# Kernel optimization log

Hardware: AMD Instinct MI355X
Metric: run time of the kernel (lower is better)

Reference implementation:

```python
import jax, jax.numpy as jnp
import numpy as np
import math

D_MODEL = 1024
N_HEADS = 16
SEQ = 1024
BATCH = 4


def setup_inputs() -> dict:
    key = jax.random.key(0)
    ks = jax.random.split(key, 13)
    s = 1.0 / math.sqrt(D_MODEL)  # keep logits in a sane range
    return {
        "x": jax.random.normal(ks[0], (BATCH, SEQ, D_MODEL), jnp.float32),
        "Wq": jax.random.normal(ks[1], (D_MODEL, D_MODEL), jnp.float32) * s,
        "bq": jnp.zeros((D_MODEL,), jnp.float32),
        "Wk": jax.random.normal(ks[2], (D_MODEL, D_MODEL), jnp.float32) * s,
        "bk": jnp.zeros((D_MODEL,), jnp.float32),
        "Wv": jax.random.normal(ks[3], (D_MODEL, D_MODEL), jnp.float32) * s,
        "bv": jnp.zeros((D_MODEL,), jnp.float32),
        "Wo": jax.random.normal(ks[4], (D_MODEL, D_MODEL), jnp.float32) * s,
        "bo": jnp.zeros((D_MODEL,), jnp.float32),
        "Wimp": jax.random.normal(ks[5], (N_HEADS, D_MODEL), jnp.float32) * s,
        "bimp": jnp.zeros((N_HEADS,), jnp.float32),
        "k_ema": jax.random.normal(ks[6], (SEQ, D_MODEL), jnp.float32),
        "v_ema": jax.random.normal(ks[7], (SEQ, D_MODEL), jnp.float32),
    }


def reference(x, Wq, bq, Wk, bk, Wv, bv, Wo, bo, Wimp, bimp, k_ema, v_ema):
    B, S, D = x.shape
    H = Wimp.shape[0]
    hd = D // H

    def proj(W, b):
        # [B,S,D] -> [B,H,S,hd]
        return (x @ W.T + b).reshape(B, S, H, hd).transpose(0, 2, 1, 3)

    q = proj(Wq, bq)
    k = proj(Wk, bk)
    v = proj(Wv, bv)

    scores = jnp.einsum("bhqd,bhkd->bhqk", q, k) / math.sqrt(hd)

    # importance bias: outer-sum of per-head key/value importance vectors
    k_imp = (k_ema[:S] @ Wimp.T + bimp).T  # [H, S]
    v_imp = (v_ema[:S] @ Wimp.T + bimp).T  # [H, S]
    bias = 0.5 * (k_imp[:, :, None] + v_imp[:, None, :])  # [H, S, S]
    scores = scores + 0.1 * bias[None]

    # causal mask (torch masks before bias add; -inf + finite == -inf, so equivalent)
    causal = jnp.triu(jnp.ones((S, S), bool), k=1)
    scores = jnp.where(causal, -jnp.inf, scores)

    attn = jax.nn.softmax(scores, axis=-1)
    out = jnp.einsum("bhqk,bhkd->bhqd", attn, v)
    out = out.transpose(0, 2, 1, 3).reshape(B, S, D)
    return out @ Wo.T + bo
```

## Files before the change

kernel.cpp:

```cpp
#include <hip/hip_runtime.h>
#include <hip/hip_bf16.h>
#include <math.h>

#define D_MODEL 1024
#define SEQ     1024
#define BATCH   4
#define NHEADS  16
#define HD      64

#define QSC 0.18033688f
#define BSC 0.072134752f

typedef __bf16 bf16x8 __attribute__((ext_vector_type(8)));
typedef __bf16 bf16x4 __attribute__((ext_vector_type(4)));
typedef float  f32x4  __attribute__((ext_vector_type(4)));

__device__ __forceinline__ f32x4 mfma16(bf16x8 a, bf16x8 b, f32x4 c) {
  return __builtin_amdgcn_mfma_f32_16x16x32_bf16(a, b, c, 0, 0, 0);
}

__device__ __forceinline__ void async16(__bf16* lds, const __bf16* g) {
  __builtin_amdgcn_global_load_lds(g, lds, 16, 0, 0);
}

__device__ __forceinline__ float fexp2(float x) {
  float r;
  asm volatile("v_exp_f32 %0, %1" : "=v"(r) : "v"(x));
  return r;
}

__global__ __launch_bounds__(256) void prep_kernel(
    const float* __restrict__ x,
    const float* __restrict__ Wq, const float* __restrict__ Wk,
    const float* __restrict__ Wv, const float* __restrict__ Wo,
    const float* __restrict__ v_ema,
    const float* __restrict__ Wimp, const float* __restrict__ bimp,
    __bf16* __restrict__ x_bf, __bf16* __restrict__ wq_bf, __bf16* __restrict__ wk_bf,
    __bf16* __restrict__ wv_bf, __bf16* __restrict__ wo_bf,
    float* __restrict__ vimp) {
  const int bid = blockIdx.x;
  const int tid = threadIdx.x;
  if (bid < 4096) {
    int i = bid * 256 + tid;
    float4 v = ((const float4*)x)[i];
    bf16x4 o; o[0] = (__bf16)v.x; o[1] = (__bf16)v.y; o[2] = (__bf16)v.z; o[3] = (__bf16)v.w;
    ((bf16x4*)x_bf)[i] = o;
  } else if (bid < 8192) {
    int i = (bid - 4096) * 256 + tid;
    int sel = i >> 18;
    int j = i & 262143;
    const float* s = (sel == 0) ? Wq : (sel == 1) ? Wk : (sel == 2) ? Wv : Wo;
    __bf16* d      = (sel == 0) ? wq_bf : (sel == 1) ? wk_bf : (sel == 2) ? wv_bf : wo_bf;
    float4 v = ((const float4*)s)[j];
    bf16x4 o; o[0] = (__bf16)v.x; o[1] = (__bf16)v.y; o[2] = (__bf16)v.z; o[3] = (__bf16)v.w;
    ((bf16x4*)d)[j] = o;
  } else {
    const int s    = (bid - 8192) * 4 + (tid >> 6);
    const int lane = tid & 63;
    const float4* ve = (const float4*)(v_ema + (size_t)s * D_MODEL);
    float acc0 = 0.f, acc1 = 0.f, acc2 = 0.f, acc3 = 0.f;
    float acc4 = 0.f, acc5 = 0.f, acc6 = 0.f, acc7 = 0.f;
    float acc8 = 0.f, acc9 = 0.f, accA = 0.f, accB = 0.f;
    float accC = 0.f, accD = 0.f, accE = 0.f, accF = 0.f;
    #pragma unroll
    for (int i = 0; i < 4; i++) {
      const int c = lane + i * 64;
      float4 v = ve[c];
      #define VIMP_H(H, ACC)                                                     \
        {                                                                        \
          float4 w = ((const float4*)(Wimp + (H) * D_MODEL))[c];                 \
          ACC += v.x * w.x + v.y * w.y + v.z * w.z + v.w * w.w;                  \
        }
      VIMP_H(0, acc0)  VIMP_H(1, acc1)  VIMP_H(2, acc2)  VIMP_H(3, acc3)
      VIMP_H(4, acc4)  VIMP_H(5, acc5)  VIMP_H(6, acc6)  VIMP_H(7, acc7)
      VIMP_H(8, acc8)  VIMP_H(9, acc9)  VIMP_H(10, accA) VIMP_H(11, accB)
      VIMP_H(12, accC) VIMP_H(13, accD) VIMP_H(14, accE) VIMP_H(15, accF)
      #undef VIMP_H
    }
    #define VIMP_RED(ACC)                                                        \
      for (int mm = 32; mm >= 1; mm >>= 1) ACC += __shfl_xor(ACC, mm);
    VIMP_RED(acc0) VIMP_RED(acc1) VIMP_RED(acc2) VIMP_RED(acc3)
    VIMP_RED(acc4) VIMP_RED(acc5) VIMP_RED(acc6) VIMP_RED(acc7)
    VIMP_RED(acc8) VIMP_RED(acc9) VIMP_RED(accA) VIMP_RED(accB)
    VIMP_RED(accC) VIMP_RED(accD) VIMP_RED(accE) VIMP_RED(accF)
    #undef VIMP_RED
    if (lane == 0) {
      vimp[0  * SEQ + s] = acc0 + bimp[0];  vimp[1  * SEQ + s] = acc1 + bimp[1];
      vimp[2  * SEQ + s] = acc2 + bimp[2];  vimp[3  * SEQ + s] = acc3 + bimp[3];
      vimp[4  * SEQ + s] = acc4 + bimp[4];  vimp[5  * SEQ + s] = acc5 + bimp[5];
      vimp[6  * SEQ + s] = acc6 + bimp[6];  vimp[7  * SEQ + s] = acc7 + bimp[7];
      vimp[8  * SEQ + s] = acc8 + bimp[8];  vimp[9  * SEQ + s] = acc9 + bimp[9];
      vimp[10 * SEQ + s] = accA + bimp[10]; vimp[11 * SEQ + s] = accB + bimp[11];
      vimp[12 * SEQ + s] = accC + bimp[12]; vimp[13 * SEQ + s] = accD + bimp[13];
      vimp[14 * SEQ + s] = accE + bimp[14]; vimp[15 * SEQ + s] = accF + bimp[15];
    }
  }
}

__global__ __launch_bounds__(256) void gemm_qkv(
    const __bf16* __restrict__ A,
    const __bf16* __restrict__ Wq, const __bf16* __restrict__ Wk, const __bf16* __restrict__ Wv,
    const float* __restrict__ bq, const float* __restrict__ bk, const float* __restrict__ bv,
    __bf16* __restrict__ qo, __bf16* __restrict__ kp, __bf16* __restrict__ vp) {
  const int id = blockIdx.x + (blockIdx.y << 4);
  const int xcd = id & 7;
  const int j = id >> 3;
  const int by = (j & 3) * 8 + xcd;
  const int bx = j >> 2;

  __shared__ __bf16 As[2 * 8192];
  __shared__ __bf16 Ws[3][2 * 4096];

  const int tid = threadIdx.x;
  const int w = tid >> 6, l = tid & 63;
  const int quad = l >> 4, l16 = l & 15;
  const int wy = w >> 1, wx = w & 1;
  const int row0 = by * 128;
  const int col0 = bx * 64;

  const f32x4 fzero = {0.f, 0.f, 0.f, 0.f};
  f32x4 aq[4][2], ak[4][2], av[4][2];
  #pragma unroll
  for (int i = 0; i < 4; i++)
    #pragma unroll
    for (int jj = 0; jj < 2; jj++) { aq[i][jj] = fzero; ak[i][jj] = fzero; av[i][jj] = fzero; }

  const int rk = tid >> 3;
  const int csw = (((tid & 7) ^ (rk & 7)) * 8);
  const int tid8 = tid * 8;
  const __bf16* aS = A  + (size_t)(row0 + rk) * D_MODEL + csw;
  const __bf16* qS = Wq + (size_t)(col0 + rk) * D_MODEL + csw;
  const __bf16* kS = Wk + (size_t)(col0 + rk) * D_MODEL + csw;
  const __bf16* vS = Wv + (size_t)(col0 + rk) * D_MODEL + csw;

  const int pch0 = ((0 * 4 + quad) ^ (l16 & 7)) * 8;
  const int pch1 = ((1 * 4 + quad) ^ (l16 & 7)) * 8;

  #pragma unroll
  for (int p = 0; p < 4; ++p)
    async16(&As[p * 2048 + tid8], aS + (size_t)p * 32 * D_MODEL);
  #pragma unroll
  for (int p = 0; p < 2; ++p) {
    async16(&Ws[0][p * 2048 + tid8], qS + (size_t)p * 32 * D_MODEL);
    async16(&Ws[1][p * 2048 + tid8], kS + (size_t)p * 32 * D_MODEL);
    async16(&Ws[2][p * 2048 + tid8], vS + (size_t)p * 32 * D_MODEL);
  }

  #pragma unroll 2
  for (int t = 0; t < 16; ++t) {
    const int rbA = (t & 1) << 13;
    const int rbW = (t & 1) << 12;
    if (t < 15) {
      const int sbA = ((t + 1) & 1) << 13;
      const int sbW = ((t + 1) & 1) << 12;
      const size_t kk = (size_t)(t + 1) * 64;
      #pragma unroll
      for (int p = 0; p < 4; ++p)
        async16(&As[sbA + p * 2048 + tid8], aS + (size_t)p * 32 * D_MODEL + kk);
      #pragma unroll
      for (int p = 0; p < 2; ++p) {
        async16(&Ws[0][sbW + p * 2048 + tid8], qS + (size_t)p * 32 * D_MODEL + kk);
        async16(&Ws[1][sbW + p * 2048 + tid8], kS + (size_t)p * 32 * D_MODEL + kk);
        async16(&Ws[2][sbW + p * 2048 + tid8], vS + (size_t)p * 32 * D_MODEL + kk);
      }
      asm volatile("s_waitcnt vmcnt(10)" ::: "memory");
    } else {
      asm volatile("s_waitcnt vmcnt(0)" ::: "memory");
    }
    __builtin_amdgcn_s_barrier();
    #pragma unroll
    for (int ks = 0; ks < 2; ++ks) {
      const int pch = ks ? pch1 : pch0;
      bf16x8 af[4], qf[2], kf[2], vf[2];
      #pragma unroll
      for (int mi = 0; mi < 4; mi++)
        af[mi] = *(const bf16x8*)&As[rbA + (wy * 64 + mi * 16 + l16) * 64 + pch];
      #pragma unroll
      for (int ni = 0; ni < 2; ni++) {
        const int wrow = (wx * 32 + ni * 16 + l16) * 64 + pch;
        qf[ni] = *(const bf16x8*)&Ws[0][rbW + wrow];
        kf[ni] = *(const bf16x8*)&Ws[1][rbW + wrow];
        vf[ni] = *(const bf16x8*)&Ws[2][rbW + wrow];
      }
      #pragma unroll
      for (int mi = 0; mi < 4; mi++)
        #pragma unroll
        for (int ni = 0; ni < 2; ni++) {
          aq[mi][ni] = mfma16(af[mi], qf[ni], aq[mi][ni]);
          ak[mi][ni] = mfma16(kf[ni], af[mi], ak[mi][ni]);
          av[mi][ni] = mfma16(af[mi], vf[ni], av[mi][ni]);
        }
    }
    __builtin_amdgcn_s_barrier();
  }

  #pragma unroll
  for (int ni = 0; ni < 2; ni++) {
    const int col = col0 + wx * 32 + ni * 16 + l16;
    const float bqv = bq[col];
    #pragma unroll
    for (int mi = 0; mi < 4; mi++) {
      const int row = row0 + wy * 64 + mi * 16 + quad * 4;
      #pragma unroll
      for (int r = 0; r < 4; r++)
        qo[(size_t)(row + r) * D_MODEL + col] = (__bf16)((aq[mi][ni][r] + bqv) * QSC);
    }
  }
  #pragma unroll
  for (int ni = 0; ni < 2; ni++) {
    const int wcolbase = col0 + wx * 32 + ni * 16 + quad * 4;
    const float4 b4 = *(const float4*)&bk[wcolbase];
    const float bb[4] = {b4.x, b4.y, b4.z, b4.w};
    #pragma unroll
    for (int mi = 0; mi < 4; mi++) {
      const int token = row0 + wy * 64 + mi * 16 + l16;
      const int bh = (token >> 10) * 16 + (wcolbase >> 6);
      const int colp = ((wcolbase & 63) + ((token & 7) << 3)) & 63;
      union { __bf16 hh[4]; uint2 uu; } pk;
      #pragma unroll
      for (int r = 0; r < 4; r++) pk.hh[r] = (__bf16)(ak[mi][ni][r] + bb[r]);
      *(uint2*)(kp + ((size_t)bh * SEQ + (token & 1023)) * HD + colp) = pk.uu;
    }
  }
  #pragma unroll
  for (int ni = 0; ni < 2; ni++) {
    const int col = col0 + wx * 32 + ni * 16 + l16;
    const float bvv = bv[col];
    #pragma unroll
    for (int mi = 0; mi < 4; mi++) {
      const int token = row0 + wy * 64 + mi * 16 + quad * 4;
      const int bh = (token >> 10) * 16 + (col >> 6);
      const int chk = (token >> 6) & 15;
      const int keyp = ((token & 63) + ((col & 7) << 3)) & 63;
      const size_t base = (((size_t)bh * 16 + chk) * 64 + (col & 63)) * 64 + keyp;
      union { __bf16 hh[4]; uint2 uu; } pk;
      #pragma unroll
      for (int r = 0; r < 4; r++) pk.hh[r] = (__bf16)(av[mi][ni][r] + bvv);
      *(uint2*)(vp + base) = pk.uu;
    }
  }
}

__global__ __launch_bounds__(256) void gemm_o(
    const __bf16* __restrict__ A, const __bf16* __restrict__ W,
    const float* __restrict__ bias, float* __restrict__ out) {
  const int id = blockIdx.x + (blockIdx.y << 4);
  const int xcd = id & 7;
  const int j = id >> 3;
  const int by = (j & 3) * 8 + xcd;
  const int bx = j >> 2;

  __shared__ __bf16 As[2 * 8192];
  __shared__ __bf16 Bs[2 * 4096];

  const int tid = threadIdx.x;
  const int w = tid >> 6, l = tid & 63;
  const int quad = l >> 4, l16 = l & 15;
  const int wy = w >> 1, wx = w & 1;
  const int row0 = by * 128;
  const int col0 = bx * 64;

  const f32x4 fzero = {0.f, 0.f, 0.f, 0.f};
  f32x4 acc[4][2];
  for (int i = 0; i < 4; i++)
    for (int jj = 0; jj < 2; jj++) acc[i][jj] = fzero;

  const int rk = tid >> 3;
  const int csw = (((tid & 7) ^ (rk & 7)) * 8);
  const int tid8 = tid * 8;
  const __bf16* aS = A + (size_t)(row0 + rk) * D_MODEL + csw;
  const __bf16* bS = W + (size_t)(col0 + rk) * D_MODEL + csw;

  const int pch0 = ((0 * 4 + quad) ^ (l16 & 7)) * 8;
  const int pch1 = ((1 * 4 + quad) ^ (l16 & 7)) * 8;

  #pragma unroll
  for (int p = 0; p < 4; ++p)
    async16(&As[p * 2048 + tid8], aS + (size_t)p * 32 * D_MODEL);
  #pragma unroll
  for (int p = 0; p < 2; ++p)
    async16(&Bs[p * 2048 + tid8], bS + (size_t)p * 32 * D_MODEL);

  #pragma unroll 2
  for (int t = 0; t < 16; ++t) {
    const int rbA = (t & 1) << 13;
    const int rbB = (t & 1) << 12;
    if (t < 15) {
      const int sbA = ((t + 1) & 1) << 13;
      const int sbB = ((t + 1) & 1) << 12;
      const size_t kk = (size_t)(t + 1) * 64;
      #pragma unroll
      for (int p = 0; p < 4; ++p)
        async16(&As[sbA + p * 2048 + tid8], aS + (size_t)p * 32 * D_MODEL + kk);
      #pragma unroll
      for (int p = 0; p < 2; ++p)
        async16(&Bs[sbB + p * 2048 + tid8], bS + (size_t)p * 32 * D_MODEL + kk);
      asm volatile("s_waitcnt vmcnt(6)" ::: "memory");
    } else {
      asm volatile("s_waitcnt vmcnt(0)" ::: "memory");
    }
    __builtin_amdgcn_s_barrier();
    #pragma unroll
    for (int ks = 0; ks < 2; ++ks) {
      const int pch = ks ? pch1 : pch0;
      bf16x8 af[4], bfr[2];
      #pragma unroll
      for (int mi = 0; mi < 4; mi++) af[mi]  = *(const bf16x8*)&As[rbA + (wy * 64 + mi * 16 + l16) * 64 + pch];
      #pragma unroll
      for (int ni = 0; ni < 2; ni++) bfr[ni] = *(const bf16x8*)&Bs[rbB + (wx * 32 + ni * 16 + l16) * 64 + pch];
      #pragma unroll
      for (int mi = 0; mi < 4; mi++)
        #pragma unroll
        for (int ni = 0; ni < 2; ni++)
          acc[mi][ni] = mfma16(af[mi], bfr[ni], acc[mi][ni]);
    }
    __builtin_amdgcn_s_barrier();
  }

  #pragma unroll
  for (int ni = 0; ni < 2; ni++) {
    const int col = col0 + wx * 32 + ni * 16 + l16;
    const float bv = bias[col];
    #pragma unroll
    for (int mi = 0; mi < 4; mi++) {
      const int row = row0 + wy * 64 + mi * 16 + quad * 4;
      #pragma unroll
      for (int r = 0; r < 4; r++)
        out[(size_t)(row + r) * D_MODEL + col] = acc[mi][ni][r] + bv;
    }
  }
}

__global__ __launch_bounds__(256, 2) void attn_kernel(
    const __bf16* __restrict__ Qb, const __bf16* __restrict__ Kp,
    const __bf16* __restrict__ Vp, const float* __restrict__ vimp,
    __bf16* __restrict__ Ob) {
  const int id = blockIdx.x;
  const int bh = id & 63;
  const int gg = id >> 6;
  const int b = bh >> 4, h = bh & 15;
  const int tid = threadIdx.x;
  const int wave = tid >> 6, lane = tid & 63;
  const int quad = lane >> 4, l16 = lane & 15;

  __shared__ __bf16 Kl[3][4096];
  __shared__ __bf16 Vl[3][4096];
  __shared__ __bf16 Ps[4][16][72];

  const __bf16* kbase = Kp + (size_t)bh * (SEQ * HD);
  const __bf16* vbase = Vp + (size_t)bh * (SEQ * HD);
  const float* vimpH = vimp + h * SEQ;

  const int rot0 = ((quad + (l16 & 7)) & 7) * 8;
  const int rot1 = ((quad + 4 + (l16 & 7)) & 7) * 8;
  const int frow = l16 * 64;

  const int g0 = gg, g1 = 15 - gg;

  const int qrow0 = g0 * 64 + wave * 16 + l16;
  const int qrow1 = g1 * 64 + wave * 16 + l16;
  const __bf16* qp0 = Qb + (size_t)(b * SEQ + qrow0) * D_MODEL + h * HD;
  const __bf16* qp1 = Qb + (size_t)(b * SEQ + qrow1) * D_MODEL + h * HD;
  bf16x8 qA0 = *(const bf16x8*)(qp0 + quad * 8);
  bf16x8 qA1 = *(const bf16x8*)(qp0 + 32 + quad * 8);
  bf16x8 qB0 = *(const bf16x8*)(qp1 + quad * 8);
  bf16x8 qB1 = *(const bf16x8*)(qp1 + 32 + quad * 8);

  async16(&Kl[0][tid * 8], kbase + tid * 8);
  async16(&Kl[0][2048 + tid * 8], kbase + 2048 + tid * 8);
  async16(&Vl[0][tid * 8], vbase + tid * 8);
  async16(&Vl[0][2048 + tid * 8], vbase + 2048 + tid * 8);
  async16(&Kl[1][tid * 8], kbase + 4096 + tid * 8);
  async16(&Kl[1][2048 + tid * 8], kbase + 4096 + 2048 + tid * 8);
  async16(&Vl[1][tid * 8], vbase + 4096 + tid * 8);
  async16(&Vl[1][2048 + tid * 8], vbase + 4096 + 2048 + tid * 8);

  float l0 = 0.f, l1 = 0.f;
  f32x4 o0[4], o1[4];
  #pragma unroll
  for (int td = 0; td < 4; td++) {
    o0[td][0] = 0.f; o0[td][1] = 0.f; o0[td][2] = 0.f; o0[td][3] = 0.f;
    o1[td][0] = 0.f; o1[td][1] = 0.f; o1[td][2] = 0.f; o1[td][3] = 0.f;
  }

  #pragma unroll 1
  for (int c = 0; c <= g1; ++c) {
    const int buf = c % 3;
    if (c < g1) asm volatile("s_waitcnt vmcnt(4)" ::: "memory");
    else        asm volatile("s_waitcnt vmcnt(0)" ::: "memory");
    __builtin_amdgcn_s_barrier();
    const int kc = c * 64;
    float4 vi[4];
    #pragma unroll
    for (int t = 0; t < 4; t++) vi[t] = *(const float4*)(vimpH + kc + t * 16 + quad * 4);
    __builtin_amdgcn_sched_barrier(0);
    if (c + 2 <= g1) {
      const int nb = (c + 2) % 3;
      const __bf16* gk = kbase + (size_t)(c + 2) * 4096;
      const __bf16* gv = vbase + (size_t)(c + 2) * 4096;
      async16(&Kl[nb][tid * 8], gk + tid * 8);
      async16(&Kl[nb][2048 + tid * 8], gk + 2048 + tid * 8);
      async16(&Vl[nb][tid * 8], gv + tid * 8);
      async16(&Vl[nb][2048 + tid * 8], gv + 2048 + tid * 8);
    }
    __builtin_amdgcn_sched_barrier(0);

    bf16x8 kf0[4], kf1[4], vfr0[4], vfr1[4];
    #pragma unroll
    for (int t = 0; t < 4; t++) {
      kf0[t] = *(const bf16x8*)&Kl[buf][t * 1024 + frow + rot0];
      kf1[t] = *(const bf16x8*)&Kl[buf][t * 1024 + frow + rot1];
    }
    #pragma unroll
    for (int td = 0; td < 4; td++) {
      vfr0[td] = *(const bf16x8*)&Vl[buf][td * 1024 + frow + rot0];
      vfr1[td] = *(const bf16x8*)&Vl[buf][td * 1024 + frow + rot1];
    }
    const f32x4 fz = {0.f, 0.f, 0.f, 0.f};

    {
      f32x4 sacc[4];
      __builtin_amdgcn_s_setprio(1);
      #pragma unroll
      for (int t = 0; t < 4; t++) {
        sacc[t] = mfma16(kf0[t], qB0, fz);
        sacc[t] = mfma16(kf1[t], qB1, sacc[t]);
      }
      __builtin_amdgcn_s_setprio(0);
      float p[4][4];
      float lsum = 0.f;
      #pragma unroll
      for (int t = 0; t < 4; t++) {
        const float vib[4] = {vi[t].x, vi[t].y, vi[t].z, vi[t].w};
        if (c == g1) {
          #pragma unroll
          for (int r = 0; r < 4; r++) {
            float pp = fexp2(sacc[t][r] + BSC * vib[r]);
            pp = (kc + t * 16 + quad * 4 + r <= qrow1) ? pp : 0.f;
            p[t][r] = pp;
            lsum += pp;
          }
        } else {
          #pragma unroll
          for (int r = 0; r < 4; r++) {
            float pp = fexp2(sacc[t][r] + BSC * vib[r]);
            p[t][r] = pp;
            lsum += pp;
          }
        }
      }
      l1 += lsum;
      #pragma unroll
      for (int t = 0; t < 4; t++) {
        union { __bf16 hh[4]; uint2 uu; } pk;
        #pragma unroll
        for (int r = 0; r < 4; r++) pk.hh[r] = (__bf16)p[t][r];
        *(uint2*)&Ps[wave][l16][t * 16 + quad * 4] = pk.uu;
      }
      bf16x8 pf0 = *(const bf16x8*)&Ps[wave][l16][quad * 8];
      bf16x8 pf1 = *(const bf16x8*)&Ps[wave][l16][32 + quad * 8];
      __builtin_amdgcn_s_setprio(1);
      #pragma unroll
      for (int td = 0; td < 4; td++) {
        o1[td] = mfma16(vfr0[td], pf0, o1[td]);
        o1[td] = mfma16(vfr1[td], pf1, o1[td]);
      }
      __builtin_amdgcn_s_setprio(0);
    }

    if (c <= g0) {
      f32x4 sacc[4];
      __builtin_amdgcn_s_setprio(1);
      #pragma unroll
      for (int t = 0; t < 4; t++) {
        sacc[t] = mfma16(kf0[t], qA0, fz);
        sacc[t] = mfma16(kf1[t], qA1, sacc[t]);
      }
      __builtin_amdgcn_s_setprio(0);
      float p[4][4];
      float lsum = 0.f;
      #pragma unroll
      for (int t = 0; t < 4; t++) {
        const float vib[4] = {vi[t].x, vi[t].y, vi[t].z, vi[t].w};
        if (c == g0) {
          #pragma unroll
          for (int r = 0; r < 4; r++) {
            float pp = fexp2(sacc[t][r] + BSC * vib[r]);
            pp = (kc + t * 16 + quad * 4 + r <= qrow0) ? pp : 0.f;
            p[t][r] = pp;
            lsum += pp;
          }
        } else {
          #pragma unroll
          for (int r = 0; r < 4; r++) {
            float pp = fexp2(sacc[t][r] + BSC * vib[r]);
            p[t][r] = pp;
            lsum += pp;
          }
        }
      }
      l0 += lsum;
      #pragma unroll
      for (int t = 0; t < 4; t++) {
        union { __bf16 hh[4]; uint2 uu; } pk;
        #pragma unroll
        for (int r = 0; r < 4; r++) pk.hh[r] = (__bf16)p[t][r];
        *(uint2*)&Ps[wave][l16][t * 16 + quad * 4] = pk.uu;
      }
      bf16x8 pf0 = *(const bf16x8*)&Ps[wave][l16][quad * 8];
      bf16x8 pf1 = *(const bf16x8*)&Ps[wave][l16][32 + quad * 8];
      __builtin_amdgcn_s_setprio(1);
      #pragma unroll
      for (int td = 0; td < 4; td++) {
        o0[td] = mfma16(vfr0[td], pf0, o0[td]);
        o0[td] = mfma16(vfr1[td], pf1, o0[td]);
      }
      __builtin_amdgcn_s_setprio(0);
      if (c == g0) {
        float L = l0;
        L += __shfl_xor(L, 16);
        L += __shfl_xor(L, 32);
        const float il = 1.0f / L;
        __bf16* op = Ob + (size_t)(b * SEQ + qrow0) * D_MODEL + h * HD;
        #pragma unroll
        for (int td = 0; td < 4; td++) {
          union { __bf16 hh[4]; uint2 uu; } pk;
          #pragma unroll
          for (int r = 0; r < 4; r++) pk.hh[r] = (__bf16)(o0[td][r] * il);
          *(uint2*)(op + td * 16 + quad * 4) = pk.uu;
        }
      }
    }
  }

  float L = l1;
  L += __shfl_xor(L, 16);
  L += __shfl_xor(L, 32);
  const float il = 1.0f / L;
  __bf16* op = Ob + (size_t)(b * SEQ + qrow1) * D_MODEL + h * HD;
  #pragma unroll
  for (int td = 0; td < 4; td++) {
    union { __bf16 hh[4]; uint2 uu; } pk;
    #pragma unroll
    for (int r = 0; r < 4; r++) pk.hh[r] = (__bf16)(o1[td][r] * il);
    *(uint2*)(op + td * 16 + quad * 4) = pk.uu;
  }
}

extern "C" void kernel_launch(void* const* d_in, const int* in_sizes, int n_in,
                              void* d_out, int out_size, void* d_ws, size_t ws_size,
                              hipStream_t stream) {
  const float* x     = (const float*)d_in[0];
  const float* Wq    = (const float*)d_in[1];
  const float* bq    = (const float*)d_in[2];
  const float* Wk    = (const float*)d_in[3];
  const float* bk    = (const float*)d_in[4];
  const float* Wv    = (const float*)d_in[5];
  const float* bv    = (const float*)d_in[6];
  const float* Wo    = (const float*)d_in[7];
  const float* bo    = (const float*)d_in[8];
  const float* Wimp  = (const float*)d_in[9];
  const float* bimp  = (const float*)d_in[10];
  const float* v_ema = (const float*)d_in[12];
  float* out = (float*)d_out;

  char* ws = (char*)d_ws;
  __bf16* x_bf  = (__bf16*)(ws);
  __bf16* wq_bf = (__bf16*)(ws + (8ull  << 20));
  __bf16* wk_bf = (__bf16*)(ws + (10ull << 20));
  __bf16* wv_bf = (__bf16*)(ws + (12ull << 20));
  __bf16* wo_bf = (__bf16*)(ws + (14ull << 20));
  __bf16* q_bf  = (__bf16*)(ws + (16ull << 20));
  __bf16* kp_bf = (__bf16*)(ws + (24ull << 20));
  __bf16* vp_bf = (__bf16*)(ws + (32ull << 20));
  __bf16* a_bf  = (__bf16*)(ws + (40ull << 20));
  float*  vimp  = (float*)(ws + (48ull << 20));

  prep_kernel<<<8448, 256, 0, stream>>>(
      x, Wq, Wk, Wv, Wo, v_ema, Wimp, bimp,
      x_bf, wq_bf, wk_bf, wv_bf, wo_bf, vimp);

  gemm_qkv<<<dim3(16, 32), 256, 0, stream>>>(
      x_bf, wq_bf, wk_bf, wv_bf, bq, bk, bv, q_bf, kp_bf, vp_bf);

  attn_kernel<<<dim3(512), 256, 0, stream>>>(
      q_bf, kp_bf, vp_bf, vimp, a_bf);

  gemm_o<<<dim3(16, 32), 256, 0, stream>>>(a_bf, wo_bf, bo, out);
}
```

Before: 180.9 us.

## Load QKV weight fragments directly into registers, bypassing LDS; reorder attention block mapping

In the fused QKV projection GEMM, weight tiles for Wq/Wk/Wv are no longer staged through shared memory. Each lane loads its MFMA B-fragments from global memory into a double-buffered register array, prefetched one k-step ahead. This cuts LDS traffic and LDS footprint but raises register pressure and relies on less-coalesced per-lane global loads; the vmcnt wait is adjusted. Separately, the attention kernel permutes the query-group index to change how causal work is spread across blocks.

```diff
diff --git a/kernel.cpp b/kernel.cpp
--- a/kernel.cpp
+++ b/kernel.cpp
@@ -109,7 +109,6 @@
   const int bx = j >> 2;
 
   __shared__ __bf16 As[2 * 8192];
-  __shared__ __bf16 Ws[3][2 * 4096];
 
   const int tid = threadIdx.x;
   const int w = tid >> 6, l = tid & 63;
@@ -128,42 +127,42 @@
   const int rk = tid >> 3;
   const int csw = (((tid & 7) ^ (rk & 7)) * 8);
   const int tid8 = tid * 8;
-  const __bf16* aS = A  + (size_t)(row0 + rk) * D_MODEL + csw;
-  const __bf16* qS = Wq + (size_t)(col0 + rk) * D_MODEL + csw;
-  const __bf16* kS = Wk + (size_t)(col0 + rk) * D_MODEL + csw;
-  const __bf16* vS = Wv + (size_t)(col0 + rk) * D_MODEL + csw;
+  const __bf16* aS = A + (size_t)(row0 + rk) * D_MODEL + csw;
+
+  const size_t wrow0 = (size_t)(col0 + wx * 32 + l16) * D_MODEL + quad * 8;
+  const __bf16* qW = Wq + wrow0;
+  const __bf16* kW = Wk + wrow0;
+  const __bf16* vW = Wv + wrow0;
 
   const int pch0 = ((0 * 4 + quad) ^ (l16 & 7)) * 8;
   const int pch1 = ((1 * 4 + quad) ^ (l16 & 7)) * 8;
 
+  bf16x8 wf[2][12];
+  #define WLOAD(BUF, KT)                                                          \
+    _Pragma("unroll") for (int ni = 0; ni < 2; ++ni)                              \
+      _Pragma("unroll") for (int ks = 0; ks < 2; ++ks) {                          \
+        const size_t off = (size_t)ni * 16 * D_MODEL + ks * 32 + (size_t)(KT) * 64; \
+        wf[BUF][0 + ni * 2 + ks] = *(const bf16x8*)(qW + off);                    \
+        wf[BUF][4 + ni * 2 + ks] = *(const bf16x8*)(kW + off);                    \
+        wf[BUF][8 + ni * 2 + ks] = *(const bf16x8*)(vW + off);                    \
+      }
+
   #pragma unroll
   for (int p = 0; p < 4; ++p)
     async16(&As[p * 2048 + tid8], aS + (size_t)p * 32 * D_MODEL);
-  #pragma unroll
-  for (int p = 0; p < 2; ++p) {
-    async16(&Ws[0][p * 2048 + tid8], qS + (size_t)p * 32 * D_MODEL);
-    async16(&Ws[1][p * 2048 + tid8], kS + (size_t)p * 32 * D_MODEL);
-    async16(&Ws[2][p * 2048 + tid8], vS + (size_t)p * 32 * D_MODEL);
-  }
+  WLOAD(0, 0)
 
   #pragma unroll 2
   for (int t = 0; t < 16; ++t) {
     const int rbA = (t & 1) << 13;
-    const int rbW = (t & 1) << 12;
+    const int cb = t & 1, nbuf = cb ^ 1;
     if (t < 15) {
-      const int sbA = ((t + 1) & 1) << 13;
-      const int sbW = ((t + 1) & 1) << 12;
       const size_t kk = (size_t)(t + 1) * 64;
       #pragma unroll
       for (int p = 0; p < 4; ++p)
-        async16(&As[sbA + p * 2048 + tid8], aS + (size_t)p * 32 * D_MODEL + kk);
-      #pragma unroll
-      for (int p = 0; p < 2; ++p) {
-        async16(&Ws[0][sbW + p * 2048 + tid8], qS + (size_t)p * 32 * D_MODEL + kk);
-        async16(&Ws[1][sbW + p * 2048 + tid8], kS + (size_t)p * 32 * D_MODEL + kk);
-        async16(&Ws[2][sbW + p * 2048 + tid8], vS + (size_t)p * 32 * D_MODEL + kk);
-      }
-      asm volatile("s_waitcnt vmcnt(10)" ::: "memory");
+        async16(&As[((t + 1) & 1) * 8192 + p * 2048 + tid8], aS + (size_t)p * 32 * D_MODEL + kk);
+      WLOAD(nbuf, t + 1)
+      asm volatile("s_waitcnt vmcnt(16)" ::: "memory");
     } else {
       asm volatile("s_waitcnt vmcnt(0)" ::: "memory");
     }
@@ -171,24 +170,17 @@
     #pragma unroll
     for (int ks = 0; ks < 2; ++ks) {
       const int pch = ks ? pch1 : pch0;
-      bf16x8 af[4], qf[2], kf[2], vf[2];
+      bf16x8 af[4];
       #pragma unroll
       for (int mi = 0; mi < 4; mi++)
         af[mi] = *(const bf16x8*)&As[rbA + (wy * 64 + mi * 16 + l16) * 64 + pch];
-      #pragma unroll
-      for (int ni = 0; ni < 2; ni++) {
-        const int wrow = (wx * 32 + ni * 16 + l16) * 64 + pch;
-        qf[ni] = *(const bf16x8*)&Ws[0][rbW + wrow];
-        kf[ni] = *(const bf16x8*)&Ws[1][rbW + wrow];
-        vf[ni] = *(const bf16x8*)&Ws[2][rbW + wrow];
-      }
       #pragma unroll
       for (int mi = 0; mi < 4; mi++)
         #pragma unroll
         for (int ni = 0; ni < 2; ni++) {
-          aq[mi][ni] = mfma16(af[mi], qf[ni], aq[mi][ni]);
-          ak[mi][ni] = mfma16(kf[ni], af[mi], ak[mi][ni]);
-          av[mi][ni] = mfma16(af[mi], vf[ni], av[mi][ni]);
+          aq[mi][ni] = mfma16(af[mi], wf[cb][0 + ni * 2 + ks], aq[mi][ni]);
+          ak[mi][ni] = mfma16(wf[cb][4 + ni * 2 + ks], af[mi], ak[mi][ni]);
+          av[mi][ni] = mfma16(af[mi], wf[cb][8 + ni * 2 + ks], av[mi][ni]);
         }
     }
     __builtin_amdgcn_s_barrier();
@@ -239,6 +231,7 @@
       *(uint2*)(vp + base) = pk.uu;
     }
   }
+  #undef WLOAD
 }
 
 __global__ __launch_bounds__(256) void gemm_o(
@@ -337,7 +330,8 @@
     __bf16* __restrict__ Ob) {
   const int id = blockIdx.x;
   const int bh = id & 63;
-  const int gg = id >> 6;
+  const int ggi = id >> 6;
+  const int gg = ggi ^ ((ggi & 4) ? 3 : 0);
   const int b = bh >> 4, h = bh & 15;
   const int tid = threadIdx.x;
   const int wave = tid >> 6, lane = tid & 63;
```

After: 293.9 us. +62.5%, slower.
